# Performance work log

Measured on AMD Instinct MI355X. Metric: run time of the kernel, lower is better.

Reference implementation:

```python
import jax, jax.numpy as jnp
import numpy as np

N_BINS = 64
INPUT_DIM = 8
R = 1.2
BOUND = 10.0
BETA = 1e-06
N = 2097152


def _mesh_and_elmt():
    m = N_BINS / 2
    idx = jnp.arange(N_BINS + 1, dtype=jnp.float32) - m
    x1L = BOUND * (R - 1.0) / (R ** m - 1.0)
    xr = (1.0 - R ** jnp.abs(idx)) / (1.0 - R)
    xr = jnp.where(idx >= 0, x1L * xr, -x1L * xr)
    xr = (xr + BOUND) / (2.0 * BOUND)
    mesh = jnp.concatenate([jnp.zeros((1,), jnp.float32), xr[1:-1], jnp.ones((1,), jnp.float32)])  # [n_bins+1]
    elmt = mesh[1:] - mesh[:-1]  # [n_bins]
    return mesh, elmt


def _pdf_normalize(p, elmt):
    # pdf: [n_bins+1, d]; F_ref: [n_bins, d] cumulative bin integrals
    p0 = jnp.full((1, INPUT_DIM), BETA, jnp.float32)
    ep = jnp.exp(p)
    px = ep * ((elmt[:-1] + elmt[1:]) / 2.0)[:, None]
    scale = (1.0 - (elmt[0] + elmt[-1]) * BETA / 2.0) / jnp.sum(px, 0, keepdims=True)
    px = scale * ep
    pdf = jnp.concatenate([p0, px, p0], 0)
    cell = (pdf[:-1] + pdf[1:]) / 2.0 * elmt[:, None]  # [n_bins, d]
    F_ref = jnp.concatenate([jnp.zeros((1, INPUT_DIM), jnp.float32),
                             jnp.cumsum(cell, 0)[:N_BINS - 1]], 0)
    return pdf, F_ref


def setup_inputs() -> dict:
    key = jax.random.key(0)
    k1, k2 = jax.random.split(key)
    x = jax.random.normal(k1, (N, INPUT_DIM), dtype=jnp.float32)
    logdet = jnp.zeros((N, 1), dtype=jnp.float32)
    p = jax.random.normal(k2, (N_BINS - 1, INPUT_DIM), dtype=jnp.float32)
    return {"x": x, "logdet": logdet, "p": p}


def reference(x, logdet, p):
    mesh, elmt = _mesh_and_elmt()
    pdf, F_ref = _pdf_normalize(p, elmt)

    xs = (x + BOUND) / (2.0 * BOUND)  # [N, d] in [0,1] for covered points
    k = jnp.searchsorted(mesh, xs, side='right') - 1  # [N, d]
    cover = (k >= 0) & (k <= N_BINS - 1)
    k = jnp.clip(k, 0, N_BINS - 1)
    col = jnp.arange(INPUT_DIM)[None, :]

    v1 = pdf[k, col]            # [N, d]
    v2 = pdf[k + 1, col]
    xm = xs - mesh[k]
    h = elmt[k]
    F_pre = F_ref[k, col]

    y = jnp.where(cover, F_pre + xm * xm / 2.0 * (v2 - v1) / h + xm * v1, xs)
    dld = jnp.where(cover, xm * (v2 - v1) / h + v1, 1.0)
    logdet = logdet + jnp.sum(jnp.log(dld), -1, keepdims=True)

    y = y * 2.0 * BOUND - BOUND
    y = jnp.where(y > BOUND, BETA * (y - BOUND) + BOUND, y)
    logdet = logdet + jnp.sum(jnp.log(jnp.where(y > BOUND, BETA, 1.0)), -1, keepdims=True)
    y = jnp.where(y < -BOUND, BETA * (y + BOUND) - BOUND, y)
    logdet = logdet + jnp.sum(jnp.log(jnp.where(y < -BOUND, BETA, 1.0)), -1, keepdims=True)
    return y, logdet
```

## Files before the change

kernel.cpp:

```cpp
#include <hip/hip_runtime.h>
#include <hip/hip_bf16.h>
#include <math.h>

#define NDIM   8
#define NBINS  64
#define LOG_BETA   (-13.815510557964274f)
#define LN2F       0.69314718055994531f
#define ALPHA      34.0821892f
#define INV_LOG2R  3.80178401692393f

__global__ __launch_bounds__(256, 8) void cdfq_fused(const float* __restrict__ x,
                                                     const float* __restrict__ logdet_in,
                                                     const float* __restrict__ p,
                                                     float* __restrict__ y_out,
                                                     float* __restrict__ ld_out,
                                                     int n)
{
    __shared__ float  mesh[65];
    __shared__ float  elmt[64];
    __shared__ float  sc[NDIM];
    __shared__ float  pdfs[NDIM][65];
    __shared__ float4 stbl[NDIM * NBINS];

    const int t  = threadIdx.x;
    const int T  = gridDim.x * blockDim.x;
    const int i0 = blockIdx.x * blockDim.x + t;
    const int G  = 2 * n;
    const int iters = G / T;
    const float4* xv4 = (const float4*)x;

    float4 Xc; float Lc;
    if (iters > 0) {
        Xc = xv4[i0];
        Lc = logdet_in[i0 >> 1];
    }
    __builtin_amdgcn_sched_barrier(0);

    if (t < 65) {
        float fidx = (float)t - 32.0f;
        float a = fabsf(fidx);
        float x1L = 2.0f / (powf(1.2f, 32.0f) - 1.0f);
        float xr = x1L * (powf(1.2f, a) - 1.0f) / 0.2f;
        xr = (fidx >= 0.0f) ? xr : -xr;
        xr = (xr + 10.0f) / 20.0f;
        if (t == 0)  xr = 0.0f;
        if (t == 64) xr = 1.0f;
        mesh[t] = xr;
    }
    for (int idx = t; idx < 63 * NDIM; idx += 256) {
        int d = idx & 7, k = idx >> 3;
        pdfs[d][k + 1] = expf(p[k * NDIM + d]);
    }
    if (t < NDIM) { pdfs[t][0] = 1e-6f; pdfs[t][64] = 1e-6f; }
    __syncthreads();
    if (t < 64) elmt[t] = mesh[t + 1] - mesh[t];
    __syncthreads();

    if (t < 64) {
        for (int d = 0; d < NDIM; ++d) {
            float w = 0.0f;
            if (t < 63) w = pdfs[d][t + 1] * 0.5f * (elmt[t] + elmt[t + 1]);
            for (int off = 32; off > 0; off >>= 1) w += __shfl_down(w, off);
            if (t == 0) sc[d] = (1.0f - (elmt[0] + elmt[63]) * 5e-7f) / w;
        }
    }
    __syncthreads();
    for (int idx = t; idx < 63 * NDIM; idx += 256) {
        int d = idx & 7, k = idx >> 3;
        pdfs[d][k + 1] *= sc[d];
    }
    __syncthreads();
    if (t < 64) {
        for (int d = 0; d < NDIM; ++d) {
            float c0 = 0.5f * (pdfs[d][t] + pdfs[d][t + 1]) * elmt[t];
            float v = c0;
            for (int off = 1; off < 64; off <<= 1) {
                float w = __shfl_up(v, off);
                if (t >= off) v += w;
            }
            float Fpre = v - c0;
            float v1 = pdfs[d][t];
            float v2 = pdfs[d][t + 1];
            stbl[d * 64 + t] = make_float4(v1, (v2 - v1) / elmt[t], Fpre, mesh[t]);
        }
    }
    __syncthreads();

    auto body = [&](float4 X, float Lin, int g) {
        const int q     = g >> 1;
        const int dbase = (g & 1) << 2;
        float xd[4] = {X.x, X.y, X.z, X.w};
        float yd[4], dd[4];
        float extra = 0.0f;

#pragma unroll
        for (int dl = 0; dl < 4; ++dl) {
            float xo = xd[dl];
            float xs = fmaf(xo, 0.05f, 0.5f);
            float u  = fabsf(xo);
            float gg = __log2f(fmaf(ALPHA, u, 1.0f)) * INV_LOG2R;
            int jp = (int)fminf(gg, 31.0f);
            int jn = (int)ceilf(fminf(gg, 32.0f));
            int k  = (xo >= 0.0f) ? (32 + jp) : (32 - jn);

            float4 tb = stbl[((dbase + dl) << 6) + k];
            float xm  = xs - tb.w;
            bool cov  = (xs >= 0.0f) && (xs < 1.0f);

            float yc = tb.z + xm * fmaf(0.5f * xm, tb.y, tb.x);
            float dv = fmaf(xm, tb.y, tb.x);
            float yy = cov ? yc : xs;
            dd[dl]   = cov ? dv : 1.0f;

            yy = fmaf(yy, 20.0f, -10.0f);
            if (yy > 10.0f)  { yy = fmaf(1e-6f, yy - 10.0f, 10.0f);  extra += LOG_BETA; }
            if (yy < -10.0f) { yy = fmaf(1e-6f, yy + 10.0f, -10.0f); extra += LOG_BETA; }
            yd[dl] = yy;
        }

        float l2 = __log2f(dd[0] * dd[1]) + __log2f(dd[2] * dd[3]);
        float contrib = fmaf(l2, LN2F, extra);
        float cross   = __shfl_xor(contrib, 1);

        ((float4*)y_out)[g] = make_float4(yd[0], yd[1], yd[2], yd[3]);
        if ((g & 1) == 0) ld_out[q] = Lin + contrib + cross;
    };

    for (int j = 0; j < iters; ++j) {
        float4 Xn; float Ln;
        const bool more = (j + 1 < iters);
        if (more) {
            int gx = i0 + (j + 1) * T;
            Xn = xv4[gx];
            Ln = logdet_in[gx >> 1];
        }
        __builtin_amdgcn_sched_barrier(0);

        body(Xc, Lc, i0 + j * T);

        if (more) { Xc = Xn; Lc = Ln; }
    }

    int gr = i0 + iters * T;
    if (gr < G) {
        body(xv4[gr], logdet_in[gr >> 1], gr);
    }
}

extern "C" void kernel_launch(void* const* d_in, const int* in_sizes, int n_in,
                              void* d_out, int out_size, void* d_ws, size_t ws_size,
                              hipStream_t stream) {
    const float* x      = (const float*)d_in[0];
    const float* logdet = (const float*)d_in[1];
    const float* p      = (const float*)d_in[2];

    const int n = in_sizes[1];
    float* y_out  = (float*)d_out;
    float* ld_out = (float*)d_out + (size_t)n * NDIM;

    const int block = 256;
    int grid = 2048;
    if ((long long)grid * block > 2LL * n) grid = (2 * n + block - 1) / block;
    cdfq_fused<<<grid, block, 0, stream>>>(x, logdet, p, y_out, ld_out, n);
}
```

Baseline: 138.9 us.

## Double prefetch depth and simplify per-element bin lookup and clamping math

The main loop now handles two grid-stride items per iteration and prefetches the next two, which puts more loads in flight per thread. The bin index is computed with a sign-mask XOR instead of separate ceil/floor paths, and coverage is tested on the log argument. The ±10 clamps become one branchless abs/copysign select, the four derivatives are multiplied into a single log2, and the table base pointer is hoisted. Both lanes of each pair now write the same logdet value redundantly, and the single product of derivatives could underflow or overflow where two partial products would not.

New measurement: 139.4 us. No clear change (+0.4%).

```diff
diff --git a/kernel.cpp b/kernel.cpp
--- a/kernel.cpp
+++ b/kernel.cpp
@@ -8,6 +8,7 @@
 #define LN2F       0.69314718055994531f
 #define ALPHA      34.0821892f
 #define INV_LOG2R  3.80178401692393f
+#define WMAX       341.821892f
 
 __global__ __launch_bounds__(256, 8) void cdfq_fused(const float* __restrict__ x,
                                                      const float* __restrict__ logdet_in,
@@ -29,10 +30,10 @@
     const int iters = G / T;
     const float4* xv4 = (const float4*)x;
 
-    float4 Xc; float Lc;
-    if (iters > 0) {
-        Xc = xv4[i0];
-        Lc = logdet_in[i0 >> 1];
+    float4 X0, X1; float L0, L1;
+    if (iters > 1) {
+        X0 = xv4[i0];           L0 = logdet_in[i0 >> 1];
+        X1 = xv4[i0 + T];       L1 = logdet_in[(i0 + T) >> 1];
     }
     __builtin_amdgcn_sched_barrier(0);
 
@@ -55,7 +56,6 @@
     __syncthreads();
     if (t < 64) elmt[t] = mesh[t + 1] - mesh[t];
     __syncthreads();
-
     if (t < 64) {
         for (int d = 0; d < NDIM; ++d) {
             float w = 0.0f;
@@ -86,65 +86,66 @@
     }
     __syncthreads();
 
+    const float4* tp = stbl + ((i0 & 1) << 8);
+
     auto body = [&](float4 X, float Lin, int g) {
-        const int q     = g >> 1;
-        const int dbase = (g & 1) << 2;
         float xd[4] = {X.x, X.y, X.z, X.w};
-        float yd[4], dd[4];
-        float extra = 0.0f;
+        float yd[4];
+        float prod = 1.0f, extra = 0.0f;
 
 #pragma unroll
         for (int dl = 0; dl < 4; ++dl) {
             float xo = xd[dl];
             float xs = fmaf(xo, 0.05f, 0.5f);
-            float u  = fabsf(xo);
-            float gg = __log2f(fmaf(ALPHA, u, 1.0f)) * INV_LOG2R;
-            int jp = (int)fminf(gg, 31.0f);
-            int jn = (int)ceilf(fminf(gg, 32.0f));
-            int k  = (xo >= 0.0f) ? (32 + jp) : (32 - jn);
+            float w  = fmaf(ALPHA, fabsf(xo), 1.0f);
+            float gg = __log2f(w) * INV_LOG2R;
+            int   jf = (int)fminf(gg, 31.0f);
+            int   m  = ((int)__float_as_int(xo)) >> 31;
+            int   k  = 32 + (jf ^ m);
+            bool cov = w < WMAX;
 
-            float4 tb = stbl[((dbase + dl) << 6) + k];
+            float4 tb = tp[(dl << 6) + k];
             float xm  = xs - tb.w;
-            bool cov  = (xs >= 0.0f) && (xs < 1.0f);
-
-            float yc = tb.z + xm * fmaf(0.5f * xm, tb.y, tb.x);
-            float dv = fmaf(xm, tb.y, tb.x);
-            float yy = cov ? yc : xs;
-            dd[dl]   = cov ? dv : 1.0f;
+            float yc  = fmaf(xm, fmaf(0.5f * xm, tb.y, tb.x), tb.z);
+            float dv  = fmaf(xm, tb.y, tb.x);
+            float yy  = cov ? yc : xs;
+            prod *= (cov ? dv : 1.0f);
 
             yy = fmaf(yy, 20.0f, -10.0f);
-            if (yy > 10.0f)  { yy = fmaf(1e-6f, yy - 10.0f, 10.0f);  extra += LOG_BETA; }
-            if (yy < -10.0f) { yy = fmaf(1e-6f, yy + 10.0f, -10.0f); extra += LOG_BETA; }
+            float ay = fabsf(yy);
+            bool cl  = ay > 10.0f;
+            float yl = copysignf(fmaf(1e-6f, ay, 10.0f - 1e-5f), yy);
+            yy = cl ? yl : yy;
+            extra += cl ? LOG_BETA : 0.0f;
             yd[dl] = yy;
         }
 
-        float l2 = __log2f(dd[0] * dd[1]) + __log2f(dd[2] * dd[3]);
-        float contrib = fmaf(l2, LN2F, extra);
+        float contrib = fmaf(__log2f(prod), LN2F, extra);
         float cross   = __shfl_xor(contrib, 1);
 
         ((float4*)y_out)[g] = make_float4(yd[0], yd[1], yd[2], yd[3]);
-        if ((g & 1) == 0) ld_out[q] = Lin + contrib + cross;
+        ld_out[g >> 1] = Lin + contrib + cross;
     };
 
-    for (int j = 0; j < iters; ++j) {
-        float4 Xn; float Ln;
-        const bool more = (j + 1 < iters);
+    for (int j = 0; j + 1 < iters; j += 2) {
+        float4 Xn0, Xn1; float Ln0, Ln1;
+        const bool more = (j + 3 < iters);
         if (more) {
-            int gx = i0 + (j + 1) * T;
-            Xn = xv4[gx];
-            Ln = logdet_in[gx >> 1];
+            int g2 = i0 + (j + 2) * T;
+            int g3 = i0 + (j + 3) * T;
+            Xn0 = xv4[g2]; Ln0 = logdet_in[g2 >> 1];
+            Xn1 = xv4[g3]; Ln1 = logdet_in[g3 >> 1];
         }
         __builtin_amdgcn_sched_barrier(0);
 
-        body(Xc, Lc, i0 + j * T);
+        body(X0, L0, i0 + j * T);
+        body(X1, L1, i0 + (j + 1) * T);
 
-        if (more) { Xc = Xn; Lc = Ln; }
+        if (more) { X0 = Xn0; L0 = Ln0; X1 = Xn1; L1 = Ln1; }
     }
 
-    int gr = i0 + iters * T;
-    if (gr < G) {
-        body(xv4[gr], logdet_in[gr >> 1], gr);
-    }
+    for (int g = i0 + (iters & ~1) * T; g < G; g += T)
+        body(xv4[g], logdet_in[g >> 1], g);
 }
 
 extern "C" void kernel_launch(void* const* d_in, const int* in_sizes, int n_in,
```
